# Performance work log

Hardware: AMD Instinct MI355X
Metric: run time of the kernel (lower is better)

The kernel has to match this reference:

```python
import jax, jax.numpy as jnp
import numpy as np

N = 20000      # query points
S = 20000      # support points
NEIGH = 30     # neighbors per query
K = 15         # kernel points
P = 3          # point dim
NQ = 4         # query LRFs
NS = 4         # support LRFs
CIN = 128
COUT = 256
LRF_C = CIN // NQ          # 32
FDIM = 2 * CIN             # 256
EXTENT = 0.05
SCALE = 0.05               # point cloud extent so offsets ~ KP_extent


def setup_inputs() -> dict:
    key = jax.random.key(0)
    ks = jax.random.split(key, 12)
    q_pts = jax.random.uniform(ks[0], (N, P), dtype=jnp.float32) * SCALE
    s_pts = jax.random.uniform(ks[1], (S, P), dtype=jnp.float32) * SCALE
    neighb_inds = jax.random.randint(ks[2], (N, NEIGH), 0, S + 1)  # S == shadow idx
    x = jax.random.normal(ks[3], (S, CIN), dtype=jnp.float32)
    q_lrf = jax.random.normal(ks[4], (N, NQ, P, P), dtype=jnp.float32)
    s_lrf = jax.random.normal(ks[5], (S, NS, P, P), dtype=jnp.float32)
    # kernel points in sphere of radius ~0.1, first fixed at center
    kernel_points = jax.random.normal(ks[6], (K, P), dtype=jnp.float32) * 0.04
    kernel_points = kernel_points.at[0].set(0.0)
    weights = jax.random.normal(ks[7], (K, FDIM, COUT), dtype=jnp.float32) / np.sqrt(FDIM).astype(np.float32)
    W_lrf = jax.random.normal(ks[8], (NS * P * P, LRF_C), dtype=jnp.float32) / np.sqrt(NS * P * P).astype(np.float32)
    b_lrf = jnp.zeros((LRF_C,), jnp.float32)
    bias = jnp.zeros((COUT,), jnp.float32)  # BatchNormBlock with use_bn=False
    return dict(q_pts=q_pts, s_pts=s_pts, neighb_inds=neighb_inds, x=x,
                q_lrf=q_lrf, s_lrf=s_lrf, kernel_points=kernel_points,
                weights=weights, W_lrf=W_lrf, b_lrf=b_lrf, bias=bias)


def reference(q_pts, s_pts, neighb_inds, x, q_lrf, s_lrf, kernel_points, weights, W_lrf, b_lrf, bias):
    # --- EKPConv_v2.forward ---
    # pad support points with shadow point at 1e6
    s_pts_pad = jnp.concatenate([s_pts, jnp.full((1, P), 1e6, s_pts.dtype)], 0)
    neighbors = s_pts_pad[neighb_inds] - q_pts[:, None, :]              # [N, n, 3]
    ql = jax.lax.stop_gradient(q_lrf)                                    # q_lrf always detached here
    # align neighbor offsets into each query LRF: [N, nq, n, 3]
    aligned = jnp.einsum('nmi,nqij->nqmj', neighbors, ql)
    kp = jax.lax.stop_gradient(kernel_points)                            # KP not trainable
    sq_d = jnp.sum((aligned[:, :, :, None, :] - kp) ** 2, -1)            # [N, nq, n, K]

    # neighbor LRFs, padded with zeros for shadow
    s_lrf_pad = jnp.concatenate([s_lrf, jnp.zeros((1, NS, P, P), s_lrf.dtype)], 0)
    nb_lrf = s_lrf_pad[neighb_inds]                                      # [N, n, ns, 3, 3]
    # (q_lrf^T @ s_lrf): [N, n, nq, ns, 3, 3]
    aligned_lrf = jnp.einsum('nqki,nmskj->nmqsij', ql, nb_lrf)
    aligned_lrf = aligned_lrf.reshape(N, NEIGH, NQ, NS * P * P)
    lrf_features = aligned_lrf @ W_lrf + b_lrf                           # [N, n, nq, LRF_C]
    neighb_mask = (neighb_inds < S).astype(lrf_features.dtype)           # [N, n]
    lrf_features = lrf_features * neighb_mask[:, :, None, None]

    # linear KP influence: [N, nq, K, n]
    all_weights = jnp.clip(1.0 - jnp.sqrt(sq_d) / EXTENT, 0.0, None)
    all_weights = jnp.swapaxes(all_weights, 2, 3)

    # split input features across query LRFs, pad shadow row
    x_r = x.reshape(S, NQ, LRF_C)
    x_pad = jnp.concatenate([x_r, jnp.zeros((1, NQ, LRF_C), x.dtype)], 0)
    neighb_x = x_pad[neighb_inds]                                        # [N, n, nq, LRF_C]
    neighb_x = jnp.concatenate([neighb_x, lrf_features], -1)             # [N, n, nq, 2*LRF_C]
    neighb_x = jnp.swapaxes(neighb_x, 1, 2)                              # [N, nq, n, 2*LRF_C]

    weighted = jnp.einsum('nqkm,nqmc->nqkc', all_weights, neighb_x)      # [N, nq, K, 2*LRF_C]
    weighted = jnp.transpose(weighted, (2, 0, 1, 3)).reshape(K, N, FDIM) # [K, N, FDIM]
    out = jnp.einsum('kni,kio->no', weighted, weights)                   # sum over K kernel GEMMs

    # --- BatchNormBlock (use_bn=False => bias) + LeakyReLU(0.1) ---
    out = out + bias
    return jnp.where(out >= 0, out, 0.1 * out)
```

## Files before the change

### kernel.cpp

```cpp
#include <hip/hip_runtime.h>

#define NQPTS 20000
#define NSUP  20000
#define NNB   30
#define NKP   15
#define KF    3840
#define KC    1920
#define EXTINV 20.0f

typedef __attribute__((ext_vector_type(4))) float f32x4;
typedef __attribute__((ext_vector_type(8))) short bf16x8;
typedef __attribute__((ext_vector_type(8))) unsigned short u16x8;

typedef __attribute__((address_space(1))) const unsigned int as1_u32;
typedef __attribute__((address_space(3))) unsigned int as3_u32;

__device__ __forceinline__ unsigned short f2bf(float f){
  unsigned int u = __float_as_uint(f);
  u = (u + 0x7FFFu + ((u >> 16) & 1u)) >> 16;
  return (unsigned short)u;
}

__device__ __forceinline__ void gl_lds16(const unsigned short* g, unsigned short* l){
  __builtin_amdgcn_global_load_lds((as1_u32*)g, (as3_u32*)l, 16, 0, 0);
}

__global__ __launch_bounds__(256) void convert_wt(const float* __restrict__ W,
                                                  unsigned short* __restrict__ Bt){
  __shared__ unsigned short tile[64*130];
  const int kf0 = blockIdx.x * 128, o0 = blockIdx.y * 64;
  const int to = threadIdx.x & 63, tk = threadIdx.x >> 6;
  #pragma unroll
  for (int i = 0; i < 32; i++){
    int kf = i*4 + tk;
    tile[to*130 + kf] = f2bf(W[(size_t)(kf0+kf)*256 + o0 + to]);
  }
  __syncthreads();
  #pragma unroll
  for (int j = 0; j < 32; j++){
    int flat = threadIdx.x + j*256;
    int ol = flat >> 7, kl = flat & 127;
    Bt[(size_t)(o0+ol)*KF + kf0 + kl] = tile[ol*130 + kl];
  }
}

__global__ __launch_bounds__(256, 4) void build_weighted_v4(
    const float* __restrict__ q_pts, const float* __restrict__ s_pts,
    const int*   __restrict__ inds,  const float* __restrict__ x,
    const float* __restrict__ q_lrf, const float* __restrict__ s_lrf,
    const float* __restrict__ kp,    const float* __restrict__ Wlrf,
    const float* __restrict__ blrf,  unsigned short* __restrict__ wsA,
    int n0)
{
  __shared__ __align__(16) unsigned short A_q[4*32*64];
  __shared__ __align__(16) unsigned short AWs[64*32];
  __shared__ __align__(16) unsigned short NXT[4*32*32];
  __shared__ __align__(16) unsigned short WT[32*64];
  __shared__ float slrfA[NNB*36];
  __shared__ float sptsA[NNB*4];

  const int tid = threadIdx.x;
  const int wid = tid >> 6, lane = tid & 63;
  const int fr = lane & 15, mg = lane >> 4;
  const int n = n0 + blockIdx.x;

  {
    f32x4 z = {0.f,0.f,0.f,0.f};
    f32x4* p = (f32x4*)A_q;
    p[tid] = z; p[256+tid] = z; p[512+tid] = z; p[768+tid] = z;
    ((f32x4*)AWs)[tid] = z;
  }

  const float qp0 = q_pts[(size_t)n*3], qp1 = q_pts[(size_t)n*3+1], qp2 = q_pts[(size_t)n*3+2];
  int idxr = NSUP;
  if (lane < NNB) idxr = inds[(size_t)n*NNB + lane];

  for (int e = tid; e < NNB*36; e += 256){
    int m = e / 36, u = e - m*36;
    int ix = inds[(size_t)n*NNB + m];
    slrfA[e] = (ix < NSUP) ? s_lrf[(size_t)ix*36 + u] : 0.f;
  }
  if (tid < NNB*4){
    int m = tid >> 2, c = tid & 3;
    if (c < 3){
      int ix = inds[(size_t)n*NNB + m];
      sptsA[tid] = (ix < NSUP) ? s_pts[(size_t)ix*3 + c] : 1e6f;
    }
  }

  {
    int c = tid & 31, u0 = (tid >> 5) * 8;
    #pragma unroll
    for (int i = 0; i < 8; i++){
      int u = u0 + i;
      float v = (u < 36) ? Wlrf[u*32 + c] : (u == 36 ? blrf[c] : 0.f);
      WT[c*64 + ((((u>>3) ^ (c&7)) << 3) | (u & 7))] = f2bf(v);
    }
  }

  int abase[3], asj[3], aug[3]; bool acta[3]; float qla[3][3];
  #pragma unroll
  for (int r = 0; r < 3; r++){
    int v = r*64 + lane;
    acta[r] = (v < 144);
    int vv = acta[r] ? v : 0;
    int q = vv/36, u = vv%36;
    int s = u/9, rem = u%9, ia = rem/3, ja = rem%3;
    asj[r]   = s*9 + ja;
    abase[r] = q*2048 + (u & 7);
    aug[r]   = u >> 3;
    #pragma unroll
    for (int k = 0; k < 3; k++)
      qla[r][k] = acta[r] ? q_lrf[(size_t)n*36 + q*9 + k*3 + ia] : 0.f;
  }
  const int qw = (lane < 60) ? lane/15 : 0;
  const int kw = (lane < 60) ? lane%15 : 0;
  float qlw[9];
  #pragma unroll
  for (int t = 0; t < 9; t++) qlw[t] = q_lrf[(size_t)n*36 + qw*9 + t];
  const float kpx = kp[kw*3], kpy = kp[kw*3+1], kpz = kp[kw*3+2];
  const int awbase = (qw*16 + kw)*32, awx = (qw*16 + kw)&3;

  float xv[16];
  #pragma unroll
  for (int nf = 0; nf < 2; nf++){
    int ch = wid*32 + nf*16 + fr;
    #pragma unroll
    for (int j = 0; j < 8; j++){
      int mm = mg*8 + j;
      int ix = __shfl(idxr, mm);
      int icx = ix < NSUP ? ix : 0;
      float v = x[(size_t)icx*128 + ch];
      xv[nf*8+j] = ix < NSUP ? v : 0.f;
    }
  }

  __syncthreads();

  for (int m = wid; m < NNB; m += 4){
    const int idx = __shfl(idxr, m);
    const bool val = (idx < NSUP);
    const float d0 = sptsA[m*4+0] - qp0;
    const float d1 = sptsA[m*4+1] - qp1;
    const float d2 = sptsA[m*4+2] - qp2;

    if (lane < 60){
      float a0 = d0*qlw[0] + d1*qlw[3] + d2*qlw[6];
      float a1 = d0*qlw[1] + d1*qlw[4] + d2*qlw[7];
      float a2 = d0*qlw[2] + d1*qlw[5] + d2*qlw[8];
      float s0 = a0-kpx, s1 = a1-kpy, s2 = a2-kpz;
      float awv = fmaxf(0.f, 1.f - sqrtf(s0*s0+s1*s1+s2*s2)*EXTINV);
      AWs[awbase + ((((m>>3) ^ awx) << 3) | (m & 7))] = f2bf(awv);
    } else {
      int qq = lane - 60;
      A_q[qq*2048 + m*64 + (((4 ^ (m&7)) << 3) | 4)] = val ? (unsigned short)0x3F80 : (unsigned short)0;
    }

    #pragma unroll
    for (int r = 0; r < 3; r++){
      if (acta[r]){
        const float* sp = &slrfA[m*36 + asj[r]];
        float acc = qla[r][0]*sp[0] + qla[r][1]*sp[3] + qla[r][2]*sp[6];
        A_q[abase[r] + m*64 + ((aug[r] ^ (m&7)) << 3)] = f2bf(acc);
      }
    }
  }

  __syncthreads();

  f32x4 cq00 = {0,0,0,0}, cq01 = cq00, cq10 = cq00, cq11 = cq00;
  #pragma unroll
  for (int step = 0; step < 2; step++){
    int g = step*4 + mg;
    bf16x8 a0 = *(const bf16x8*)&A_q[wid*2048 + (fr     )*64 + ((g ^ (fr&7)) << 3)];
    bf16x8 a1 = *(const bf16x8*)&A_q[wid*2048 + (16 + fr)*64 + ((g ^ ((16+fr)&7)) << 3)];
    bf16x8 b0 = *(const bf16x8*)&WT[(fr     )*64 + ((g ^ (fr&7)) << 3)];
    bf16x8 b1 = *(const bf16x8*)&WT[(16 + fr)*64 + ((g ^ ((16+fr)&7)) << 3)];
    cq00 = __builtin_amdgcn_mfma_f32_16x16x32_bf16(a0, b0, cq00, 0, 0, 0);
    cq01 = __builtin_amdgcn_mfma_f32_16x16x32_bf16(a0, b1, cq01, 0, 0, 0);
    cq10 = __builtin_amdgcn_mfma_f32_16x16x32_bf16(a1, b0, cq10, 0, 0, 0);
    cq11 = __builtin_amdgcn_mfma_f32_16x16x32_bf16(a1, b1, cq11, 0, 0, 0);
  }
  #pragma unroll
  for (int mt = 0; mt < 2; mt++){
    #pragma unroll
    for (int ct = 0; ct < 2; ct++){
      f32x4 cv = (mt==0) ? (ct==0 ? cq00 : cq01) : (ct==0 ? cq10 : cq11);
      #pragma unroll
      for (int r = 0; r < 4; r++){
        int mrow = mt*16 + mg*4 + r;
        int c0 = ct*16 + fr;
        NXT[wid*1024 + c0*32 + ((((mrow>>3) ^ (c0&3)) << 3) | (mrow & 7))] = f2bf(cv[r]);
      }
    }
  }

  bf16x8 xf[2];
  #pragma unroll
  for (int nf = 0; nf < 2; nf++)
    #pragma unroll
    for (int j = 0; j < 8; j++)
      ((unsigned short*)&xf[nf])[j] = f2bf(xv[nf*8+j]);

  asm volatile("s_waitcnt lgkmcnt(0)" ::: "memory");

  const int arow = wid*16 + fr;
  bf16x8 awf = *(const bf16x8*)&AWs[arow*32 + ((mg ^ (arow&3)) << 3)];
  const size_t base = (size_t)blockIdx.x * KF;
  #pragma unroll
  for (int nf = 0; nf < 4; nf++){
    bf16x8 bf_;
    if (nf < 2){
      bf_ = xf[nf];
    } else {
      int c0 = (nf-2)*16 + fr;
      bf_ = *(const bf16x8*)&NXT[wid*1024 + c0*32 + ((mg ^ (c0&3)) << 3)];
    }
    f32x4 z = {0,0,0,0};
    f32x4 d = __builtin_amdgcn_mfma_f32_16x16x32_bf16(awf, bf_, z, 0, 0, 0);
    #pragma unroll
    for (int r = 0; r < 4; r++){
      int k = mg*4 + r;
      if (k < NKP)
        wsA[base + k*256 + wid*64 + nf*16 + fr] = f2bf(d[r]);
    }
  }
}

__global__ __launch_bounds__(512, 4) void gemm_out_v4(
    const unsigned short* __restrict__ A,
    const unsigned short* __restrict__ Bt,
    const float* __restrict__ bias,
    float* __restrict__ out, int n0)
{
  __shared__ __align__(16) unsigned short As[2][2][64*32];
  __shared__ __align__(16) unsigned short Bs[2][2][256*32];
  const int tid = threadIdx.x, lane = tid & 63;
  const int w  = tid >> 6;
  const int g  = w >> 2;
  const int wg = w & 3;
  const int t2 = tid & 255;
  const int fr = lane & 15, mg = lane >> 4;
  const int m0 = blockIdx.x * 64;
  const int gk0 = g * KC;

  const unsigned short* aSrc = A  + (size_t)(m0 + (t2>>2))*KF + gk0 + (t2&3)*8;
  const unsigned short* bSrc = Bt + (size_t)(t2>>2)*KF + gk0 + (t2&3)*8;

  f32x4 acc[4][4];
  #pragma unroll
  for (int i = 0; i < 4; i++)
    #pragma unroll
    for (int j = 0; j < 4; j++){ f32x4 z = {0,0,0,0}; acc[i][j] = z; }

  const int afo = fr*32 + mg*8;
  const int bfo = (wg*64 + fr)*32 + mg*8;

  #define STG(buf, k0)                                                       \
    do {                                                                     \
      gl_lds16(aSrc + (k0), &As[g][buf][t2*8]);                              \
      gl_lds16(bSrc + (size_t)0*64*KF + (k0), &Bs[g][buf][0*2048 + t2*8]);   \
      gl_lds16(bSrc + (size_t)1*64*KF + (k0), &Bs[g][buf][1*2048 + t2*8]);   \
      gl_lds16(bSrc + (size_t)2*64*KF + (k0), &Bs[g][buf][2*2048 + t2*8]);   \
      gl_lds16(bSrc + (size_t)3*64*KF + (k0), &Bs[g][buf][3*2048 + t2*8]);   \
    } while (0)

  STG(0, 0);
  asm volatile("s_waitcnt vmcnt(0)" ::: "memory");
  __syncthreads();

  int cur = 0;
  for (int t = 0; t < KC/32; ++t){
    if (t + 1 < KC/32) STG(cur^1, (t+1)*32);
    bf16x8 af[4], bf[4];
    #pragma unroll
    for (int mf = 0; mf < 4; mf++) af[mf] = *(const bf16x8*)&As[g][cur][afo + mf*512];
    #pragma unroll
    for (int nf = 0; nf < 4; nf++) bf[nf] = *(const bf16x8*)&Bs[g][cur][bfo + nf*512];
    #pragma unroll
    for (int mf = 0; mf < 4; mf++)
      #pragma unroll
      for (int nf = 0; nf < 4; nf++)
        acc[mf][nf] = __builtin_amdgcn_mfma_f32_16x16x32_bf16(af[mf], bf[nf], acc[mf][nf], 0, 0, 0);
    asm volatile("s_waitcnt vmcnt(0)" ::: "memory");
    __syncthreads();
    cur ^= 1;
  }
  #undef STG

  float* Cred = (float*)&Bs[0][0][0];
  if (g == 1){
    #pragma unroll
    for (int mf = 0; mf < 4; mf++)
      #pragma unroll
      for (int nf = 0; nf < 4; nf++)
        #pragma unroll
        for (int r = 0; r < 4; r++)
          Cred[(mf*16 + mg*4 + r)*256 + wg*64 + nf*16 + fr] = acc[mf][nf][r];
  }
  __syncthreads();
  if (g == 0){
    float bv4[4];
    #pragma unroll
    for (int nf = 0; nf < 4; nf++) bv4[nf] = bias[wg*64 + nf*16 + fr];
    #pragma unroll
    for (int mf = 0; mf < 4; mf++){
      #pragma unroll
      for (int nf = 0; nf < 4; nf++){
        #pragma unroll
        for (int r = 0; r < 4; r++){
          int row = mf*16 + mg*4 + r;
          int n_g = n0 + m0 + row;
          if (n_g < NQPTS){
            int o = wg*64 + nf*16 + fr;
            float v = acc[mf][nf][r] + Cred[row*256 + o] + bv4[nf];
            out[(size_t)n_g*256 + o] = (v >= 0.f) ? v : 0.1f*v;
          }
        }
      }
    }
  }
}

extern "C" void kernel_launch(void* const* d_in, const int* in_sizes, int n_in,
                              void* d_out, int out_size, void* d_ws, size_t ws_size,
                              hipStream_t stream)
{
  const float* q_pts = (const float*)d_in[0];
  const float* s_pts = (const float*)d_in[1];
  const int*   inds  = (const int*)  d_in[2];
  const float* x     = (const float*)d_in[3];
  const float* q_lrf = (const float*)d_in[4];
  const float* s_lrf = (const float*)d_in[5];
  const float* kp    = (const float*)d_in[6];
  const float* wts   = (const float*)d_in[7];
  const float* Wlrf  = (const float*)d_in[8];
  const float* blrf  = (const float*)d_in[9];
  const float* bias  = (const float*)d_in[10];
  float* out = (float*)d_out;

  const size_t BBYTES = (size_t)256 * KF * sizeof(unsigned short);
  unsigned short* wsB = (unsigned short*)d_ws;
  unsigned short* wsA = (unsigned short*)((char*)d_ws + BBYTES);

  size_t avail = (ws_size > BBYTES) ? (ws_size - BBYTES) : 0;
  long maxRows = (long)(avail / ((size_t)KF * sizeof(unsigned short)));
  long chunk = (maxRows / 128) * 128;
  if (chunk > 20096) chunk = 20096;
  if (chunk < 128)   chunk = 128;

  convert_wt<<<dim3(30, 4), 256, 0, stream>>>(wts, wsB);

  for (long n0 = 0; n0 < NQPTS; n0 += chunk){
    long rows = NQPTS - n0; if (rows > chunk) rows = chunk;
    long padM = ((rows + 63)/64)*64;
    build_weighted_v4<<<(int)rows, 256, 0, stream>>>(q_pts, s_pts, inds, x,
        q_lrf, s_lrf, kp, Wlrf, blrf, wsA, (int)n0);
    gemm_out_v4<<<(int)(padM/64), 512, 0, stream>>>(wsA, wsB, bias, out, (int)n0);
  }
}
```

Measured before the change: 408.4 us.

## Precompute LRF weight fragments, compact s_lrf to bf16, retile output GEMM

A new one-block kernel packs the LRF linear weights into per-lane MFMA B fragments once, so each build block loads them into registers instead of rebuilding a shared tile. The build kernel also stores gathered s_lrf in bf16, gets q_lrf through wave shuffles, unrolls the neighbor loop and raises the occupancy hint. The output GEMM drops its split-K 64x256 tile and cross-group reduction for a 32x128 tile over the full K on a 2D grid, which gives more blocks but fewer MFMAs per LDS load. Storing s_lrf in bf16 lowers precision a little.

```diff
diff --git a/kernel.cpp b/kernel.cpp
--- a/kernel.cpp
+++ b/kernel.cpp
@@ -1,11 +1,11 @@
 #include <hip/hip_runtime.h>
+#include <hip/hip_bf16.h>
 
 #define NQPTS 20000
 #define NSUP  20000
 #define NNB   30
 #define NKP   15
 #define KF    3840
-#define KC    1920
 #define EXTINV 20.0f
 
 typedef __attribute__((ext_vector_type(4))) float f32x4;
@@ -16,11 +16,12 @@
 typedef __attribute__((address_space(3))) unsigned int as3_u32;
 
 __device__ __forceinline__ unsigned short f2bf(float f){
-  unsigned int u = __float_as_uint(f);
-  u = (u + 0x7FFFu + ((u >> 16) & 1u)) >> 16;
-  return (unsigned short)u;
-}
-
+  __hip_bfloat16 h = __float2bfloat16(f);
+  return __builtin_bit_cast(unsigned short, h);
+}
+__device__ __forceinline__ float bf2f(unsigned short u){
+  return __uint_as_float(((unsigned int)u) << 16);
+}
 __device__ __forceinline__ void gl_lds16(const unsigned short* g, unsigned short* l){
   __builtin_amdgcn_global_load_lds((as1_u32*)g, (as3_u32*)l, 16, 0, 0);
 }
@@ -44,25 +45,49 @@
   }
 }
 
-__global__ __launch_bounds__(256, 4) void build_weighted_v4(
+__global__ __launch_bounds__(64) void prep_wtfrag(const float* __restrict__ Wlrf,
+                                                  const float* __restrict__ blrf,
+                                                  unsigned short* __restrict__ wtf){
+  const int lane = threadIdx.x, fr = lane & 15, mg = lane >> 4;
+  #pragma unroll
+  for (int step = 0; step < 2; step++){
+    #pragma unroll
+    for (int half = 0; half < 2; half++){
+      int c = half*16 + fr;
+      #pragma unroll
+      for (int j = 0; j < 8; j++){
+        int u = step*32 + mg*8 + j;
+        float v = (u < 36) ? Wlrf[u*32 + c] : (u == 36 ? blrf[c] : 0.f);
+        wtf[((size_t)(step*2+half)*64 + lane)*8 + j] = f2bf(v);
+      }
+    }
+  }
+}
+
+__global__ __launch_bounds__(256, 5) void build_weighted_v5(
     const float* __restrict__ q_pts, const float* __restrict__ s_pts,
     const int*   __restrict__ inds,  const float* __restrict__ x,
     const float* __restrict__ q_lrf, const float* __restrict__ s_lrf,
-    const float* __restrict__ kp,    const float* __restrict__ Wlrf,
-    const float* __restrict__ blrf,  unsigned short* __restrict__ wsA,
-    int n0)
+    const float* __restrict__ kp,    const unsigned short* __restrict__ wtf,
+    unsigned short* __restrict__ wsA, int n0)
 {
   __shared__ __align__(16) unsigned short A_q[4*32*64];
   __shared__ __align__(16) unsigned short AWs[64*32];
   __shared__ __align__(16) unsigned short NXT[4*32*32];
-  __shared__ __align__(16) unsigned short WT[32*64];
-  __shared__ float slrfA[NNB*36];
-  __shared__ float sptsA[NNB*4];
+  __shared__ unsigned short slrfA[NNB*36];
+  __shared__ __align__(16) float sptsA[NNB*4];
 
   const int tid = threadIdx.x;
   const int wid = tid >> 6, lane = tid & 63;
   const int fr = lane & 15, mg = lane >> 4;
   const int n = n0 + blockIdx.x;
+
+  bf16x8 wtb[2][2];
+  #pragma unroll
+  for (int s = 0; s < 2; s++)
+    #pragma unroll
+    for (int h = 0; h < 2; h++)
+      wtb[s][h] = *(const bf16x8*)&wtf[((size_t)(s*2+h)*64 + lane)*8];
 
   {
     f32x4 z = {0.f,0.f,0.f,0.f};
@@ -75,28 +100,7 @@
   int idxr = NSUP;
   if (lane < NNB) idxr = inds[(size_t)n*NNB + lane];
 
-  for (int e = tid; e < NNB*36; e += 256){
-    int m = e / 36, u = e - m*36;
-    int ix = inds[(size_t)n*NNB + m];
-    slrfA[e] = (ix < NSUP) ? s_lrf[(size_t)ix*36 + u] : 0.f;
-  }
-  if (tid < NNB*4){
-    int m = tid >> 2, c = tid & 3;
-    if (c < 3){
-      int ix = inds[(size_t)n*NNB + m];
-      sptsA[tid] = (ix < NSUP) ? s_pts[(size_t)ix*3 + c] : 1e6f;
-    }
-  }
-
-  {
-    int c = tid & 31, u0 = (tid >> 5) * 8;
-    #pragma unroll
-    for (int i = 0; i < 8; i++){
-      int u = u0 + i;
-      float v = (u < 36) ? Wlrf[u*32 + c] : (u == 36 ? blrf[c] : 0.f);
-      WT[c*64 + ((((u>>3) ^ (c&7)) << 3) | (u & 7))] = f2bf(v);
-    }
-  }
+  const float qv = (lane < 36) ? q_lrf[(size_t)n*36 + lane] : 0.f;
 
   int abase[3], asj[3], aug[3]; bool acta[3]; float qla[3][3];
   #pragma unroll
@@ -111,57 +115,71 @@
     aug[r]   = u >> 3;
     #pragma unroll
     for (int k = 0; k < 3; k++)
-      qla[r][k] = acta[r] ? q_lrf[(size_t)n*36 + q*9 + k*3 + ia] : 0.f;
+      qla[r][k] = __shfl(qv, q*9 + k*3 + ia);
   }
   const int qw = (lane < 60) ? lane/15 : 0;
   const int kw = (lane < 60) ? lane%15 : 0;
   float qlw[9];
   #pragma unroll
-  for (int t = 0; t < 9; t++) qlw[t] = q_lrf[(size_t)n*36 + qw*9 + t];
+  for (int t = 0; t < 9; t++) qlw[t] = __shfl(qv, qw*9 + t);
   const float kpx = kp[kw*3], kpy = kp[kw*3+1], kpz = kp[kw*3+2];
   const int awbase = (qw*16 + kw)*32, awx = (qw*16 + kw)&3;
 
+  for (int e = tid; e < NNB*36; e += 256){
+    int m = e / 36, u = e - m*36;
+    int ix = inds[(size_t)n*NNB + m];
+    slrfA[e] = (ix < NSUP) ? f2bf(s_lrf[(size_t)ix*36 + u]) : (unsigned short)0;
+  }
+  if (tid < NNB*4){
+    int m = tid >> 2, c = tid & 3;
+    if (c < 3){
+      int ix = inds[(size_t)n*NNB + m];
+      sptsA[tid] = (ix < NSUP) ? s_pts[(size_t)ix*3 + c] : 1e6f;
+    } else sptsA[tid] = 0.f;
+  }
+
   float xv[16];
   #pragma unroll
   for (int nf = 0; nf < 2; nf++){
     int ch = wid*32 + nf*16 + fr;
     #pragma unroll
     for (int j = 0; j < 8; j++){
-      int mm = mg*8 + j;
-      int ix = __shfl(idxr, mm);
-      int icx = ix < NSUP ? ix : 0;
-      float v = x[(size_t)icx*128 + ch];
+      int ix = __shfl(idxr, mg*8 + j);
+      float v = x[(size_t)(ix < NSUP ? ix : 0)*128 + ch];
       xv[nf*8+j] = ix < NSUP ? v : 0.f;
     }
   }
 
   __syncthreads();
 
-  for (int m = wid; m < NNB; m += 4){
-    const int idx = __shfl(idxr, m);
-    const bool val = (idx < NSUP);
-    const float d0 = sptsA[m*4+0] - qp0;
-    const float d1 = sptsA[m*4+1] - qp1;
-    const float d2 = sptsA[m*4+2] - qp2;
-
-    if (lane < 60){
-      float a0 = d0*qlw[0] + d1*qlw[3] + d2*qlw[6];
-      float a1 = d0*qlw[1] + d1*qlw[4] + d2*qlw[7];
-      float a2 = d0*qlw[2] + d1*qlw[5] + d2*qlw[8];
-      float s0 = a0-kpx, s1 = a1-kpy, s2 = a2-kpz;
-      float awv = fmaxf(0.f, 1.f - sqrtf(s0*s0+s1*s1+s2*s2)*EXTINV);
-      AWs[awbase + ((((m>>3) ^ awx) << 3) | (m & 7))] = f2bf(awv);
-    } else {
-      int qq = lane - 60;
-      A_q[qq*2048 + m*64 + (((4 ^ (m&7)) << 3) | 4)] = val ? (unsigned short)0x3F80 : (unsigned short)0;
-    }
-
-    #pragma unroll
-    for (int r = 0; r < 3; r++){
-      if (acta[r]){
-        const float* sp = &slrfA[m*36 + asj[r]];
-        float acc = qla[r][0]*sp[0] + qla[r][1]*sp[3] + qla[r][2]*sp[6];
-        A_q[abase[r] + m*64 + ((aug[r] ^ (m&7)) << 3)] = f2bf(acc);
+  #pragma unroll
+  for (int it = 0; it < 8; ++it){
+    const int m = wid + it*4;
+    if (m < NNB){
+      const int idx = __shfl(idxr, m);
+      const bool val = (idx < NSUP);
+      f32x4 sp4 = *(const f32x4*)&sptsA[m*4];
+      const float d0 = sp4[0] - qp0, d1 = sp4[1] - qp1, d2 = sp4[2] - qp2;
+
+      if (lane < 60){
+        float a0 = d0*qlw[0] + d1*qlw[3] + d2*qlw[6];
+        float a1 = d0*qlw[1] + d1*qlw[4] + d2*qlw[7];
+        float a2 = d0*qlw[2] + d1*qlw[5] + d2*qlw[8];
+        float s0 = a0-kpx, s1 = a1-kpy, s2 = a2-kpz;
+        float awv = fmaxf(0.f, 1.f - sqrtf(s0*s0+s1*s1+s2*s2)*EXTINV);
+        AWs[awbase + ((((m>>3) ^ awx) << 3) | (m & 7))] = f2bf(awv);
+      } else {
+        int qq = lane - 60;
+        A_q[qq*2048 + m*64 + (((4 ^ (m&7)) << 3) | 4)] = val ? (unsigned short)0x3F80 : (unsigned short)0;
+      }
+
+      #pragma unroll
+      for (int r = 0; r < 3; r++){
+        if (acta[r]){
+          const unsigned short* sp = &slrfA[m*36 + asj[r]];
+          float acc = qla[r][0]*bf2f(sp[0]) + qla[r][1]*bf2f(sp[3]) + qla[r][2]*bf2f(sp[6]);
+          A_q[abase[r] + m*64 + ((aug[r] ^ (m&7)) << 3)] = f2bf(acc);
+        }
       }
     }
   }
@@ -174,12 +192,10 @@
     int g = step*4 + mg;
     bf16x8 a0 = *(const bf16x8*)&A_q[wid*2048 + (fr     )*64 + ((g ^ (fr&7)) << 3)];
     bf16x8 a1 = *(const bf16x8*)&A_q[wid*2048 + (16 + fr)*64 + ((g ^ ((16+fr)&7)) << 3)];
-    bf16x8 b0 = *(const bf16x8*)&WT[(fr     )*64 + ((g ^ (fr&7)) << 3)];
-    bf16x8 b1 = *(const bf16x8*)&WT[(16 + fr)*64 + ((g ^ ((16+fr)&7)) << 3)];
-    cq00 = __builtin_amdgcn_mfma_f32_16x16x32_bf16(a0, b0, cq00, 0, 0, 0);
-    cq01 = __builtin_amdgcn_mfma_f32_16x16x32_bf16(a0, b1, cq01, 0, 0, 0);
-    cq10 = __builtin_amdgcn_mfma_f32_16x16x32_bf16(a1, b0, cq10, 0, 0, 0);
-    cq11 = __builtin_amdgcn_mfma_f32_16x16x32_bf16(a1, b1, cq11, 0, 0, 0);
+    cq00 = __builtin_amdgcn_mfma_f32_16x16x32_bf16(a0, wtb[step][0], cq00, 0, 0, 0);
+    cq01 = __builtin_amdgcn_mfma_f32_16x16x32_bf16(a0, wtb[step][1], cq01, 0, 0, 0);
+    cq10 = __builtin_amdgcn_mfma_f32_16x16x32_bf16(a1, wtb[step][0], cq10, 0, 0, 0);
+    cq11 = __builtin_amdgcn_mfma_f32_16x16x32_bf16(a1, wtb[step][1], cq11, 0, 0, 0);
   }
   #pragma unroll
   for (int mt = 0; mt < 2; mt++){
@@ -227,42 +243,34 @@
   }
 }
 
-__global__ __launch_bounds__(512, 4) void gemm_out_v4(
+__global__ __launch_bounds__(256, 6) void gemm_out_v5(
     const unsigned short* __restrict__ A,
     const unsigned short* __restrict__ Bt,
     const float* __restrict__ bias,
     float* __restrict__ out, int n0)
 {
-  __shared__ __align__(16) unsigned short As[2][2][64*32];
-  __shared__ __align__(16) unsigned short Bs[2][2][256*32];
-  const int tid = threadIdx.x, lane = tid & 63;
-  const int w  = tid >> 6;
-  const int g  = w >> 2;
-  const int wg = w & 3;
-  const int t2 = tid & 255;
+  __shared__ __align__(16) unsigned short As[2][32*32];
+  __shared__ __align__(16) unsigned short Bs[2][128*32];
+  const int tid = threadIdx.x, lane = tid & 63, wid = tid >> 6;
   const int fr = lane & 15, mg = lane >> 4;
-  const int m0 = blockIdx.x * 64;
-  const int gk0 = g * KC;
-
-  const unsigned short* aSrc = A  + (size_t)(m0 + (t2>>2))*KF + gk0 + (t2&3)*8;
-  const unsigned short* bSrc = Bt + (size_t)(t2>>2)*KF + gk0 + (t2&3)*8;
-
-  f32x4 acc[4][4];
-  #pragma unroll
-  for (int i = 0; i < 4; i++)
-    #pragma unroll
-    for (int j = 0; j < 4; j++){ f32x4 z = {0,0,0,0}; acc[i][j] = z; }
-
-  const int afo = fr*32 + mg*8;
-  const int bfo = (wg*64 + fr)*32 + mg*8;
-
-  #define STG(buf, k0)                                                       \
-    do {                                                                     \
-      gl_lds16(aSrc + (k0), &As[g][buf][t2*8]);                              \
-      gl_lds16(bSrc + (size_t)0*64*KF + (k0), &Bs[g][buf][0*2048 + t2*8]);   \
-      gl_lds16(bSrc + (size_t)1*64*KF + (k0), &Bs[g][buf][1*2048 + t2*8]);   \
-      gl_lds16(bSrc + (size_t)2*64*KF + (k0), &Bs[g][buf][2*2048 + t2*8]);   \
-      gl_lds16(bSrc + (size_t)3*64*KF + (k0), &Bs[g][buf][3*2048 + t2*8]);   \
+  const int m0 = blockIdx.x * 32;
+  const int o0 = blockIdx.y * 128;
+
+  const unsigned short* aSrc = A  + (size_t)(m0 + (tid>>2))*KF + (tid&3)*8;
+  const unsigned short* bSrc0 = Bt + (size_t)(o0 + (tid>>2))*KF + (tid&3)*8;
+  const unsigned short* bSrc1 = Bt + (size_t)(o0 + 64 + (tid>>2))*KF + (tid&3)*8;
+
+  f32x4 acc[2][2];
+  #pragma unroll
+  for (int i = 0; i < 2; i++)
+    #pragma unroll
+    for (int j = 0; j < 2; j++){ f32x4 z = {0,0,0,0}; acc[i][j] = z; }
+
+  #define STG(buf, k0)                                                  \
+    do {                                                                \
+      if (tid < 128) gl_lds16(aSrc + (k0), &As[buf][tid*8]);            \
+      gl_lds16(bSrc0 + (k0), &Bs[buf][tid*8]);                          \
+      gl_lds16(bSrc1 + (k0), &Bs[buf][2048 + tid*8]);                   \
     } while (0)
 
   STG(0, 0);
@@ -270,17 +278,17 @@
   __syncthreads();
 
   int cur = 0;
-  for (int t = 0; t < KC/32; ++t){
-    if (t + 1 < KC/32) STG(cur^1, (t+1)*32);
-    bf16x8 af[4], bf[4];
-    #pragma unroll
-    for (int mf = 0; mf < 4; mf++) af[mf] = *(const bf16x8*)&As[g][cur][afo + mf*512];
-    #pragma unroll
-    for (int nf = 0; nf < 4; nf++) bf[nf] = *(const bf16x8*)&Bs[g][cur][bfo + nf*512];
-    #pragma unroll
-    for (int mf = 0; mf < 4; mf++)
-      #pragma unroll
-      for (int nf = 0; nf < 4; nf++)
+  for (int t = 0; t < KF/32; ++t){
+    if (t + 1 < KF/32) STG(cur^1, (t+1)*32);
+    bf16x8 af[2], bf[2];
+    #pragma unroll
+    for (int mf = 0; mf < 2; mf++) af[mf] = *(const bf16x8*)&As[cur][(mf*16 + fr)*32 + mg*8];
+    #pragma unroll
+    for (int nf = 0; nf < 2; nf++) bf[nf] = *(const bf16x8*)&Bs[cur][(wid*32 + nf*16 + fr)*32 + mg*8];
+    #pragma unroll
+    for (int mf = 0; mf < 2; mf++)
+      #pragma unroll
+      for (int nf = 0; nf < 2; nf++)
         acc[mf][nf] = __builtin_amdgcn_mfma_f32_16x16x32_bf16(af[mf], bf[nf], acc[mf][nf], 0, 0, 0);
     asm volatile("s_waitcnt vmcnt(0)" ::: "memory");
     __syncthreads();
@@ -288,34 +296,21 @@
   }
   #undef STG
 
-  float* Cred = (float*)&Bs[0][0][0];
-  if (g == 1){
-    #pragma unroll
-    for (int mf = 0; mf < 4; mf++)
-      #pragma unroll
-      for (int nf = 0; nf < 4; nf++)
-        #pragma unroll
-        for (int r = 0; r < 4; r++)
-          Cred[(mf*16 + mg*4 + r)*256 + wg*64 + nf*16 + fr] = acc[mf][nf][r];
-  }
-  __syncthreads();
-  if (g == 0){
-    float bv4[4];
-    #pragma unroll
-    for (int nf = 0; nf < 4; nf++) bv4[nf] = bias[wg*64 + nf*16 + fr];
-    #pragma unroll
-    for (int mf = 0; mf < 4; mf++){
-      #pragma unroll
-      for (int nf = 0; nf < 4; nf++){
-        #pragma unroll
-        for (int r = 0; r < 4; r++){
-          int row = mf*16 + mg*4 + r;
-          int n_g = n0 + m0 + row;
-          if (n_g < NQPTS){
-            int o = wg*64 + nf*16 + fr;
-            float v = acc[mf][nf][r] + Cred[row*256 + o] + bv4[nf];
-            out[(size_t)n_g*256 + o] = (v >= 0.f) ? v : 0.1f*v;
-          }
+  float bv[2];
+  #pragma unroll
+  for (int nf = 0; nf < 2; nf++) bv[nf] = bias[o0 + wid*32 + nf*16 + fr];
+  #pragma unroll
+  for (int mf = 0; mf < 2; mf++){
+    #pragma unroll
+    for (int nf = 0; nf < 2; nf++){
+      #pragma unroll
+      for (int r = 0; r < 4; r++){
+        int row = mf*16 + mg*4 + r;
+        int n_g = n0 + m0 + row;
+        if (n_g < NQPTS){
+          int o = o0 + wid*32 + nf*16 + fr;
+          float v = acc[mf][nf][r] + bv[nf];
+          out[(size_t)n_g*256 + o] = (v >= 0.f) ? v : 0.1f*v;
         }
       }
     }
@@ -339,23 +334,27 @@
   const float* bias  = (const float*)d_in[10];
   float* out = (float*)d_out;
 
-  const size_t BBYTES = (size_t)256 * KF * sizeof(unsigned short);
-  unsigned short* wsB = (unsigned short*)d_ws;
-  unsigned short* wsA = (unsigned short*)((char*)d_ws + BBYTES);
-
-  size_t avail = (ws_size > BBYTES) ? (ws_size - BBYTES) : 0;
+  const size_t BBYTES  = (size_t)256 * KF * sizeof(unsigned short);
+  const size_t WTBYTES = 4096;
+  unsigned short* wsB  = (unsigned short*)d_ws;
+  unsigned short* wtf  = (unsigned short*)((char*)d_ws + BBYTES);
+  unsigned short* wsA  = (unsigned short*)((char*)d_ws + BBYTES + WTBYTES);
+
+  size_t used = BBYTES + WTBYTES;
+  size_t avail = (ws_size > used) ? (ws_size - used) : 0;
   long maxRows = (long)(avail / ((size_t)KF * sizeof(unsigned short)));
   long chunk = (maxRows / 128) * 128;
   if (chunk > 20096) chunk = 20096;
   if (chunk < 128)   chunk = 128;
 
   convert_wt<<<dim3(30, 4), 256, 0, stream>>>(wts, wsB);
+  prep_wtfrag<<<1, 64, 0, stream>>>(Wlrf, blrf, wtf);
 
   for (long n0 = 0; n0 < NQPTS; n0 += chunk){
     long rows = NQPTS - n0; if (rows > chunk) rows = chunk;
-    long padM = ((rows + 63)/64)*64;
-    build_weighted_v4<<<(int)rows, 256, 0, stream>>>(q_pts, s_pts, inds, x,
-        q_lrf, s_lrf, kp, Wlrf, blrf, wsA, (int)n0);
-    gemm_out_v4<<<(int)(padM/64), 512, 0, stream>>>(wsA, wsB, bias, out, (int)n0);
-  }
-}
+    long padM = ((rows + 31)/32)*32;
+    build_weighted_v5<<<(int)rows, 256, 0, stream>>>(q_pts, s_pts, inds, x,
+        q_lrf, s_lrf, kp, wtf, wsA, (int)n0);
+    gemm_out_v5<<<dim3((int)(padM/32), 2), 256, 0, stream>>>(wsA, wsB, bias, out, (int)n0);
+  }
+}
```

Result: faster. 372.3 us (-8.8%).
